# Kernel tuning notes

Hardware: AMD Instinct MI355X
Metric: run time of the kernel (lower is better)

Reference implementation:

```python
import jax, jax.numpy as jnp
import numpy as np

EPS = 1e-5
NUM_HEADS = 16
TEMP = 0.01

def _ln(x, g, b):
    m = jnp.mean(x, axis=-1, keepdims=True)
    v = jnp.var(x, axis=-1, keepdims=True)
    return (x - m) * jax.lax.rsqrt(v + EPS) * g + b

def setup_inputs() -> dict:
    key = jax.random.key(0)
    ks = jax.random.split(key, 16)
    b, l, c, ni = 4, 1024, 1024, 2
    d = c // NUM_HEADS
    s = lambda fan: 1.0 / np.sqrt(fan)
    return {
        "x_list": jax.random.normal(ks[0], (b, l, c, ni), jnp.float32),
        "w_": jax.random.normal(ks[1], (4 + ni, 1), jnp.float32),
        "qkv_w": jax.random.normal(ks[2], (3 * c, c), jnp.float32) * s(c),
        "qkv_b": jax.random.normal(ks[3], (3 * c,), jnp.float32) * 0.02,
        "proj_w": jax.random.normal(ks[4], (c, c), jnp.float32) * s(c),
        "proj_b": jax.random.normal(ks[5], (c,), jnp.float32) * 0.02,
        "nq_g": jnp.ones((d,), jnp.float32),
        "nq_b": jnp.zeros((d,), jnp.float32),
        "nk_g": jnp.ones((d,), jnp.float32),
        "nk_b": jnp.zeros((d,), jnp.float32),
        "conv_w": jax.random.normal(ks[6], (c, c), jnp.float32) * s(c),
        "conv_b": jax.random.normal(ks[7], (c,), jnp.float32) * 0.02,
        "ca1_w": jax.random.normal(ks[8], (c // 16, c), jnp.float32) * s(c),
        "ca1_b": jax.random.normal(ks[9], (c // 16,), jnp.float32) * 0.02,
        "ca2_w": jax.random.normal(ks[10], (c, c // 16), jnp.float32) * s(c // 16),
        "ca2_b": jax.random.normal(ks[11], (c,), jnp.float32) * 0.02,
        "mlp1_w": jax.random.normal(ks[12], (4 * c, c), jnp.float32) * s(c),
        "mlp1_b": jax.random.normal(ks[13], (4 * c,), jnp.float32) * 0.02,
        "mlp2_w": jax.random.normal(ks[14], (c, 4 * c), jnp.float32) * s(4 * c),
        "mlp2_b": jax.random.normal(ks[15], (c,), jnp.float32) * 0.02,
    }

def reference(x_list, w_, qkv_w, qkv_b, proj_w, proj_b, nq_g, nq_b, nk_g, nk_b,
              conv_w, conv_b, ca1_w, ca1_b, ca2_w, ca2_b, mlp1_w, mlp1_b, mlp2_w, mlp2_b):
    x = x_list[..., -1]  # [b, l, c]
    # op 0: Conv1x1Act = GELU(Linear)
    op0 = jax.nn.gelu(x @ conv_w.T + conv_b, approximate=False)
    # op 1: ChannelAttention = sigmoid(fc2(relu(fc1(x)))) * x
    op1 = jax.nn.sigmoid(jax.nn.relu(x @ ca1_w.T + ca1_b) @ ca2_w.T + ca2_b) * x
    # op 2: Identity
    op2 = x
    # op 3: MLP = fc2(GELU(fc1(x)))
    op3 = jax.nn.gelu(x @ mlp1_w.T + mlp1_b, approximate=False) @ mlp2_w.T + mlp2_b
    new = jnp.stack([op0, op1, op2, op3], axis=-1)  # [b, l, c, 4]
    xc = jnp.concatenate([x_list, new], axis=-1)    # [b, l, c, ni+4]
    w = jax.nn.softmax(w_ / TEMP, axis=0)           # [ni+4, 1]
    x = jnp.einsum('blcn,ni->blci', xc, w)[..., 0]  # [b, l, c]
    x_res = x
    # attention with per-head LayerNorm on q, k
    b_, n, c = x.shape
    d = c // NUM_HEADS
    qkv = x @ qkv_w.T + qkv_b
    q, k, v = jnp.split(qkv, 3, axis=-1)
    to_heads = lambda t: t.reshape(b_, n, NUM_HEADS, d).transpose(0, 2, 1, 3)  # [b, h, n, d]
    q, k, v = to_heads(q), to_heads(k), to_heads(v)
    q = _ln(q, nq_g, nq_b)
    k = _ln(k, nk_g, nk_b)
    score = jnp.einsum('bhnd,bhmd->bhnm', q, k) / np.sqrt(d).astype(np.float32)
    attn = jax.nn.softmax(score, axis=-1)           # [b, h, n, n]
    attn_map = attn.mean(axis=1)[:, 0, 1:]          # [b, n-1]
    out = jnp.einsum('bhnm,bhmd->bhnd', attn, v)
    out = out.transpose(0, 2, 1, 3).reshape(b_, n, c)
    out = out @ proj_w.T + proj_b + x_res
    return out, attn_map
```

## Files before the change

### kernel.cpp

```cpp
#include <hip/hip_runtime.h>
#include <hip/hip_bf16.h>

typedef __attribute__((ext_vector_type(8))) short short8;
typedef __attribute__((ext_vector_type(4))) float f32x4;

#define MROWS 4096
#define CDIM  1024
#define HEADS 16
#define DHEAD 64
#define NSEQ  1024

__device__ inline float softw(const float* __restrict__ w, int idx) {
    float m = w[0];
#pragma unroll
    for (int i = 1; i < 6; i++) m = fmaxf(m, w[i]);
    float s = 0.f, v = 0.f;
#pragma unroll
    for (int i = 0; i < 6; i++) {
        float e = __expf((w[i] - m) * 100.0f);
        s += e;
        if (i == idx) v = e;
    }
    return v / s;
}

__device__ inline float gelu_f(float x) {
    return 0.5f * x * (1.0f + erff(x * 0.70710678118654752f));
}

__global__ __launch_bounds__(256) void mix_base(
    const float* __restrict__ x_list, __hip_bfloat16* __restrict__ xb,
    float* __restrict__ am_acc)
{
    int i = blockIdx.x * 256 + threadIdx.x;
    xb[i] = __float2bfloat16(x_list[2 * (size_t)i + 1]);
    if (i < 4096) am_acc[i] = 0.f;
}

__global__ __launch_bounds__(256) void f2b(const float* __restrict__ in,
                                           __hip_bfloat16* __restrict__ out, int n)
{
    int i = blockIdx.x * 256 + threadIdx.x;
    if (i < n) out[i] = __float2bfloat16(in[i]);
}

#define BKT 32
#define LDA 40

template<int EPI, int FM, int FN>
__global__ __launch_bounds__(256) void gemm_bf16(
    const __hip_bfloat16* __restrict__ A, const __hip_bfloat16* __restrict__ W,
    const float* __restrict__ bias,
    float* __restrict__ f0, const float* __restrict__ f1,
    __hip_bfloat16* __restrict__ b0, __hip_bfloat16* __restrict__ b1,
    __hip_bfloat16* __restrict__ b2,
    const float* __restrict__ g0, const float* __restrict__ be0,
    const float* __restrict__ g1, const float* __restrict__ be1,
    const float* __restrict__ wvec, int M, int N, int K)
{
    constexpr int BMt = FM * 32;
    constexpr int BNt = FN * 32;
    constexpr int NA = BMt / 64;
    constexpr int NB = BNt / 64;
    __shared__ __hip_bfloat16 As[2][BMt * LDA];
    __shared__ __hip_bfloat16 Bs[2][BNt * LDA];
    int t = threadIdx.x;
    int n0 = blockIdx.x * BNt, m0 = blockIdx.y * BMt;
    int wave = t >> 6, lane = t & 63;
    int wr = wave >> 1, wc = wave & 1;
    int quad = lane >> 4, l16 = lane & 15;
    int r0 = t >> 2, c0 = (t & 3) * 8;

    short8 sa0[NA], sb0[NB], sa1[NA], sb1[NB];
    auto ldg = [&](int k0, short8* da, short8* db) {
#pragma unroll
        for (int i = 0; i < NA; i++)
            da[i] = *(const short8*)(A + (size_t)(m0 + r0 + 64 * i) * K + k0 + c0);
#pragma unroll
        for (int i = 0; i < NB; i++)
            db[i] = *(const short8*)(W + (size_t)(n0 + r0 + 64 * i) * K + k0 + c0);
    };
    ldg(0, sa0, sb0);
    ldg(BKT, sa1, sb1);

    f32x4 zero = {0.f, 0.f, 0.f, 0.f};
    f32x4 acc[FM][FN];
#pragma unroll
    for (int i = 0; i < FM; i++)
#pragma unroll
        for (int j = 0; j < FN; j++) acc[i][j] = zero;

    for (int k0 = 0; k0 < K; k0 += 2 * BKT) {
#pragma unroll
        for (int i = 0; i < NA; i++)
            *(short8*)&As[0][(r0 + 64 * i) * LDA + c0] = sa0[i];
#pragma unroll
        for (int i = 0; i < NB; i++)
            *(short8*)&Bs[0][(r0 + 64 * i) * LDA + c0] = sb0[i];
        __syncthreads();
        if (k0 + 2 * BKT < K) ldg(k0 + 2 * BKT, sa0, sb0);
        {
            short8 af[FM], bf[FN];
#pragma unroll
            for (int i = 0; i < FM; i++)
                af[i] = *(const short8*)&As[0][(wr * FM * 16 + i * 16 + l16) * LDA + quad * 8];
#pragma unroll
            for (int j = 0; j < FN; j++)
                bf[j] = *(const short8*)&Bs[0][(wc * FN * 16 + j * 16 + l16) * LDA + quad * 8];
#pragma unroll
            for (int i = 0; i < FM; i++)
#pragma unroll
                for (int j = 0; j < FN; j++)
                    acc[i][j] = __builtin_amdgcn_mfma_f32_16x16x32_bf16(
                        af[i], bf[j], acc[i][j], 0, 0, 0);
        }
#pragma unroll
        for (int i = 0; i < NA; i++)
            *(short8*)&As[1][(r0 + 64 * i) * LDA + c0] = sa1[i];
#pragma unroll
        for (int i = 0; i < NB; i++)
            *(short8*)&Bs[1][(r0 + 64 * i) * LDA + c0] = sb1[i];
        __syncthreads();
        if (k0 + 3 * BKT < K) ldg(k0 + 3 * BKT, sa1, sb1);
        {
            short8 af[FM], bf[FN];
#pragma unroll
            for (int i = 0; i < FM; i++)
                af[i] = *(const short8*)&As[1][(wr * FM * 16 + i * 16 + l16) * LDA + quad * 8];
#pragma unroll
            for (int j = 0; j < FN; j++)
                bf[j] = *(const short8*)&Bs[1][(wc * FN * 16 + j * 16 + l16) * LDA + quad * 8];
#pragma unroll
            for (int i = 0; i < FM; i++)
#pragma unroll
                for (int j = 0; j < FN; j++)
                    acc[i][j] = __builtin_amdgcn_mfma_f32_16x16x32_bf16(
                        af[i], bf[j], acc[i][j], 0, 0, 0);
        }
    }

    if constexpr (EPI == 1) {
        float wmx = softw(wvec, 2);
        float w0c = softw(wvec, 0);
        float w14c = softw(wvec, 1) + softw(wvec, 4);
        int colbase = n0 + wc * FN * 16;
        bool isconv = colbase < 1024;
#pragma unroll
        for (int i = 0; i < FM; i++) {
#pragma unroll
            for (int j = 0; j < FN; j++) {
                int col = colbase + j * 16 + l16;
                float bv = isconv ? bias[col] : be0[col - 1024];
#pragma unroll
                for (int r = 0; r < 4; r++) {
                    int row = m0 + wr * FM * 16 + i * 16 + quad * 4 + r;
                    float v = acc[i][j][r] + bv;
                    if (isconv) {
                        size_t idx = (size_t)row * 1024 + col;
                        float2 xl = ((const float2*)f1)[idx];
                        b0[idx] = __float2bfloat16(
                            w0c * xl.x + w14c * xl.y + wmx * gelu_f(v));
                    } else {
                        b1[(size_t)row * 4096 + (col - 1024)] =
                            __float2bfloat16(gelu_f(v));
                    }
                }
            }
        }
        return;
    }

    if constexpr (EPI == 5) {
        int colbase = n0 + wc * FN * 16;
        int portion = colbase >> 10;
        int hh = (colbase >> 6) & 15;
        float bv[FN];
#pragma unroll
        for (int j = 0; j < FN; j++) bv[j] = bias[colbase + j * 16 + l16];
        if (portion == 2) {
#pragma unroll
            for (int i = 0; i < FM; i++)
#pragma unroll
                for (int j = 0; j < FN; j++)
#pragma unroll
                    for (int r = 0; r < 4; r++) {
                        int row = m0 + wr * FM * 16 + i * 16 + quad * 4 + r;
                        int bb = row >> 10, nn = row & 1023;
                        int dd = j * 16 + l16;
                        b0[((size_t)(bb * 16 + hh) * DHEAD + dd) * NSEQ + nn] =
                            __float2bfloat16(acc[i][j][r] + bv[j]);
                    }
        } else {
            const float* g  = (portion == 0) ? g0 : g1;
            const float* be = (portion == 0) ? be0 : be1;
            __hip_bfloat16* dst = (portion == 0) ? b1 : b2;
            float gv[FN], bev[FN];
#pragma unroll
            for (int j = 0; j < FN; j++) {
                gv[j] = g[j * 16 + l16];
                bev[j] = be[j * 16 + l16];
            }
#pragma unroll
            for (int i = 0; i < FM; i++)
#pragma unroll
                for (int r = 0; r < 4; r++) {
                    float s1 = 0.f, s2 = 0.f;
#pragma unroll
                    for (int j = 0; j < FN; j++) {
                        float v = acc[i][j][r] + bv[j];
                        s1 += v; s2 += v * v;
                    }
#pragma unroll
                    for (int mk = 1; mk < 16; mk <<= 1) {
                        s1 += __shfl_xor(s1, mk, 64);
                        s2 += __shfl_xor(s2, mk, 64);
                    }
                    float mean = s1 * (1.f / 64.f);
                    float var = s2 * (1.f / 64.f) - mean * mean;
                    float rs = rsqrtf(var + 1e-5f);
                    int row = m0 + wr * FM * 16 + i * 16 + quad * 4 + r;
                    int bb = row >> 10, nn = row & 1023;
                    size_t base = ((size_t)(bb * 16 + hh) * NSEQ + nn) * DHEAD;
#pragma unroll
                    for (int j = 0; j < FN; j++)
                        dst[base + j * 16 + l16] = __float2bfloat16(
                            (acc[i][j][r] + bv[j] - mean) * rs * gv[j] + bev[j]);
                }
        }
        return;
    }

    float wmx = 0.f;
    if (EPI == 3) wmx = softw(wvec, 5);

#pragma unroll
    for (int i = 0; i < FM; i++) {
#pragma unroll
        for (int j = 0; j < FN; j++) {
            int col = n0 + wc * FN * 16 + j * 16 + l16;
            float bv = bias[col];
#pragma unroll
            for (int r = 0; r < 4; r++) {
                int row = m0 + wr * FM * 16 + i * 16 + quad * 4 + r;
                float v = acc[i][j][r] + bv;
                size_t idx = (size_t)row * N + col;
                if (EPI == 3) {
                    float tv = __bfloat162float(b0[idx]) + wmx * v;
                    b0[idx] = __float2bfloat16(tv);
                } else if (EPI == 4) {
                    f0[idx] = v + __bfloat162float(b1[idx]);
                }
            }
        }
    }
}

__global__ __launch_bounds__(256) void ca1_kernel(
    const __hip_bfloat16* __restrict__ xb, const float* __restrict__ w,
    const float* __restrict__ bias, float* __restrict__ h1)
{
    __shared__ float Xs[16 * 65];
    __shared__ float Ws[64 * 65];
    int t = threadIdx.x;
    int m0 = blockIdx.x * 16;
    int row = t >> 4, cg = t & 15;
    float acc[4] = {0.f, 0.f, 0.f, 0.f};
    for (int k0 = 0; k0 < 1024; k0 += 64) {
#pragma unroll
        for (int i = 0; i < 4; i++) {
            int e = t + i * 256; int r = e >> 6, c = e & 63;
            Xs[r * 65 + c] = __bfloat162float(xb[(size_t)(m0 + r) * 1024 + k0 + c]);
        }
#pragma unroll
        for (int i = 0; i < 16; i++) {
            int e = t + i * 256; int r = e >> 6, c = e & 63;
            Ws[r * 65 + c] = w[(size_t)r * 1024 + k0 + c];
        }
        __syncthreads();
        for (int k = 0; k < 64; k++) {
            float xv = Xs[row * 65 + k];
#pragma unroll
            for (int c = 0; c < 4; c++)
                acc[c] += xv * Ws[(cg * 4 + c) * 65 + k];
        }
        __syncthreads();
    }
#pragma unroll
    for (int c = 0; c < 4; c++)
        h1[(size_t)(m0 + row) * 64 + cg * 4 + c] =
            fmaxf(acc[c] + bias[cg * 4 + c], 0.f);
}

__global__ __launch_bounds__(256) void ca2_kernel(
    const float* __restrict__ h1, const float* __restrict__ w,
    const float* __restrict__ bias, const __hip_bfloat16* __restrict__ xb,
    __hip_bfloat16* __restrict__ xmixb, const float* __restrict__ wvec)
{
    __shared__ float Wt[256 * 65];
    __shared__ float hs[16 * 64];
    int t = threadIdx.x;
    int m0 = blockIdx.x * 16, n0 = blockIdx.y * 256;
#pragma unroll
    for (int i = 0; i < 64; i++) {
        int e = t + i * 256; int r = e >> 6, c = e & 63;
        Wt[r * 65 + c] = w[(size_t)(n0 + r) * 64 + c];
    }
#pragma unroll
    for (int i = 0; i < 4; i++) {
        int e = t + i * 256; int r = e >> 6, c = e & 63;
        hs[r * 64 + c] = h1[(size_t)(m0 + r) * 64 + c];
    }
    __syncthreads();
    int n = n0 + t;
    float bv = bias[n];
    float acc[16];
#pragma unroll
    for (int mi = 0; mi < 16; mi++) acc[mi] = bv;
    for (int k = 0; k < 64; k++) {
        float wv = Wt[t * 65 + k];
#pragma unroll
        for (int mi = 0; mi < 16; mi++) acc[mi] += hs[mi * 64 + k] * wv;
    }
    float w3 = softw(wvec, 3);
#pragma unroll
    for (int mi = 0; mi < 16; mi++) {
        size_t idx = (size_t)(m0 + mi) * 1024 + n;
        float sg = 1.f / (1.f + __expf(-acc[mi]));
        float cur = __bfloat162float(xmixb[idx]);
        xmixb[idx] = __float2bfloat16(cur + w3 * sg * __bfloat162float(xb[idx]));
    }
}

#define PSTR 72
__global__ __launch_bounds__(256) void flash_mfma(
    const __hip_bfloat16* __restrict__ qb, const __hip_bfloat16* __restrict__ kb,
    const __hip_bfloat16* __restrict__ vt, __hip_bfloat16* __restrict__ ao)
{
    __shared__ __hip_bfloat16 Plds[4][32 * PSTR];
    int bh = blockIdx.x;
    int i0 = blockIdx.y * 128;
    int b = bh >> 4, h = bh & 15;
    int t = threadIdx.x, wave = t >> 6, lane = t & 63;
    int l16 = lane & 15, quad = lane >> 4;
    const __hip_bfloat16* qbase = qb + (size_t)bh * NSEQ * DHEAD;
    const __hip_bfloat16* kbase = kb + (size_t)bh * NSEQ * DHEAD;
    const __hip_bfloat16* vbase = vt + (size_t)bh * DHEAD * NSEQ;
    __hip_bfloat16* pw = Plds[wave];
    int qrow0 = i0 + wave * 32;

    short8 aq[2][2];
#pragma unroll
    for (int ri = 0; ri < 2; ri++)
#pragma unroll
        for (int ks = 0; ks < 2; ks++)
            aq[ri][ks] = *(const short8*)(qbase +
                (size_t)(qrow0 + ri * 16 + l16) * DHEAD + ks * 32 + quad * 8);

    f32x4 zero = {0.f, 0.f, 0.f, 0.f};
    f32x4 o[2][4];
    float mrow[2][4], lrow[2][4];
#pragma unroll
    for (int ri = 0; ri < 2; ri++) {
#pragma unroll
        for (int nt = 0; nt < 4; nt++) o[ri][nt] = zero;
#pragma unroll
        for (int rr = 0; rr < 4; rr++) { mrow[ri][rr] = -1e30f; lrow[ri][rr] = 0.f; }
    }

    for (int j0 = 0; j0 < NSEQ; j0 += 64) {
        short8 bk[4][2];
#pragma unroll
        for (int jt = 0; jt < 4; jt++)
#pragma unroll
            for (int ks = 0; ks < 2; ks++)
                bk[jt][ks] = *(const short8*)(kbase +
                    (size_t)(j0 + jt * 16 + l16) * DHEAD + ks * 32 + quad * 8);
        short8 bv[4][2];
#pragma unroll
        for (int nt = 0; nt < 4; nt++)
#pragma unroll
            for (int ks = 0; ks < 2; ks++)
                bv[nt][ks] = *(const short8*)(vbase +
                    (size_t)(nt * 16 + l16) * NSEQ + j0 + ks * 32 + quad * 8);

#pragma unroll
        for (int ri = 0; ri < 2; ri++) {
            f32x4 s[4];
#pragma unroll
            for (int jt = 0; jt < 4; jt++) s[jt] = zero;
#pragma unroll
            for (int jt = 0; jt < 4; jt++)
#pragma unroll
                for (int ks = 0; ks < 2; ks++)
                    s[jt] = __builtin_amdgcn_mfma_f32_16x16x32_bf16(
                        aq[ri][ks], bk[jt][ks], s[jt], 0, 0, 0);
#pragma unroll
            for (int rr = 0; rr < 4; rr++) {
                float mx = -1e30f;
#pragma unroll
                for (int jt = 0; jt < 4; jt++) {
                    s[jt][rr] *= 0.125f;
                    mx = fmaxf(mx, s[jt][rr]);
                }
#pragma unroll
                for (int mk = 1; mk < 16; mk <<= 1) mx = fmaxf(mx, __shfl_xor(mx, mk, 64));
                float om = mrow[ri][rr];
                float nm = fmaxf(om, mx);
                float al = __expf(om - nm);
                mrow[ri][rr] = nm;
                float ss = 0.f;
#pragma unroll
                for (int jt = 0; jt < 4; jt++) {
                    float p = __expf(s[jt][rr] - nm);
                    pw[(ri * 16 + quad * 4 + rr) * PSTR + jt * 16 + l16] =
                        __float2bfloat16(p);
                    ss += p;
                }
#pragma unroll
                for (int mk = 1; mk < 16; mk <<= 1) ss += __shfl_xor(ss, mk, 64);
                lrow[ri][rr] = lrow[ri][rr] * al + ss;
#pragma unroll
                for (int nt = 0; nt < 4; nt++) o[ri][nt][rr] *= al;
            }
        }
#pragma unroll
        for (int ri = 0; ri < 2; ri++) {
            short8 ap[2];
#pragma unroll
            for (int ks = 0; ks < 2; ks++)
                ap[ks] = *(const short8*)&pw[(ri * 16 + l16) * PSTR + ks * 32 + quad * 8];
#pragma unroll
            for (int nt = 0; nt < 4; nt++)
#pragma unroll
                for (int ks = 0; ks < 2; ks++)
                    o[ri][nt] = __builtin_amdgcn_mfma_f32_16x16x32_bf16(
                        ap[ks], bv[nt][ks], o[ri][nt], 0, 0, 0);
        }
    }

#pragma unroll
    for (int ri = 0; ri < 2; ri++)
#pragma unroll
        for (int rr = 0; rr < 4; rr++) {
            float inv = 1.f / lrow[ri][rr];
            int row = qrow0 + ri * 16 + quad * 4 + rr;
#pragma unroll
            for (int nt = 0; nt < 4; nt++)
                ao[((size_t)b * NSEQ + row) * CDIM + h * 64 + nt * 16 + l16] =
                    __float2bfloat16(o[ri][nt][rr] * inv);
        }
}

__global__ __launch_bounds__(256) void attn_map_acc(
    const __hip_bfloat16* __restrict__ qf, const __hip_bfloat16* __restrict__ kf,
    float* __restrict__ am)
{
    __shared__ float q0[64];
    __shared__ float red[256];
    int bh = blockIdx.x, t = threadIdx.x;
    const __hip_bfloat16* qr = qf + (size_t)bh * NSEQ * DHEAD;
    const __hip_bfloat16* kb = kf + (size_t)bh * NSEQ * DHEAD;
    if (t < 64) q0[t] = __bfloat162float(qr[t]);
    __syncthreads();
    float s[4];
    float mx = -1e30f;
#pragma unroll
    for (int ji = 0; ji < 4; ji++) {
        int j = ji * 256 + t;
        float a = 0.f;
        for (int k = 0; k < 64; k++) a += q0[k] * __bfloat162float(kb[(size_t)j * 64 + k]);
        a *= 0.125f;
        s[ji] = a;
        mx = fmaxf(mx, a);
    }
    red[t] = mx; __syncthreads();
    for (int st = 128; st > 0; st >>= 1) {
        if (t < st) red[t] = fmaxf(red[t], red[t + st]);
        __syncthreads();
    }
    float M = red[0]; __syncthreads();
    float sum = 0.f;
#pragma unroll
    for (int ji = 0; ji < 4; ji++) { s[ji] = __expf(s[ji] - M); sum += s[ji]; }
    red[t] = sum; __syncthreads();
    for (int st = 128; st > 0; st >>= 1) {
        if (t < st) red[t] += red[t + st];
        __syncthreads();
    }
    float inv = 1.f / red[0];
    int b = bh >> 4;
#pragma unroll
    for (int ji = 0; ji < 4; ji++) {
        int j = ji * 256 + t;
        if (j > 0) atomicAdd(&am[b * 1024 + j], s[ji] * inv * (1.f / 16.f));
    }
}

__global__ __launch_bounds__(256) void attn_map_out(
    const float* __restrict__ am, float* __restrict__ out1)
{
    int i = blockIdx.x * 256 + threadIdx.x;
    if (i < 4 * 1023) {
        int b = i / 1023;
        int j = i - b * 1023 + 1;
        out1[i] = am[b * 1024 + j];
    }
}

extern "C" void kernel_launch(void* const* d_in, const int* in_sizes, int n_in,
                              void* d_out, int out_size, void* d_ws, size_t ws_size,
                              hipStream_t stream)
{
    const float* x_list = (const float*)d_in[0];
    const float* wvec   = (const float*)d_in[1];
    const float* qkv_w  = (const float*)d_in[2];
    const float* qkv_b  = (const float*)d_in[3];
    const float* proj_w = (const float*)d_in[4];
    const float* proj_b = (const float*)d_in[5];
    const float* nq_g   = (const float*)d_in[6];
    const float* nq_b   = (const float*)d_in[7];
    const float* nk_g   = (const float*)d_in[8];
    const float* nk_b   = (const float*)d_in[9];
    const float* conv_w = (const float*)d_in[10];
    const float* conv_b = (const float*)d_in[11];
    const float* ca1_w  = (const float*)d_in[12];
    const float* ca1_b  = (const float*)d_in[13];
    const float* ca2_w  = (const float*)d_in[14];
    const float* ca2_b  = (const float*)d_in[15];
    const float* mlp1_w = (const float*)d_in[16];
    const float* mlp1_b = (const float*)d_in[17];
    const float* mlp2_w = (const float*)d_in[18];
    const float* mlp2_b = (const float*)d_in[19];

    float* out0 = (float*)d_out;
    float* out1 = out0 + (size_t)4 * 1024 * 1024;

    char* ws = (char*)d_ws;
    size_t off = 0;
    auto alloc = [&](size_t bytes) -> char* {
        char* p = ws + off;
        off += (bytes + 255) & ~(size_t)255;
        return p;
    };
    __hip_bfloat16* xb     = (__hip_bfloat16*)alloc((size_t)MROWS * CDIM * 2);
    __hip_bfloat16* xmixb  = (__hip_bfloat16*)alloc((size_t)MROWS * CDIM * 2);
    float*          h1     = (float*)alloc((size_t)MROWS * 64 * 4);
    __hip_bfloat16* hb     = (__hip_bfloat16*)alloc((size_t)MROWS * 4096 * 2);
    __hip_bfloat16* qbb    = (__hip_bfloat16*)alloc((size_t)MROWS * CDIM * 2);
    __hip_bfloat16* kbb    = (__hip_bfloat16*)alloc((size_t)MROWS * CDIM * 2);
    __hip_bfloat16* vtb    = (__hip_bfloat16*)alloc((size_t)MROWS * CDIM * 2);
    __hip_bfloat16* aob    = (__hip_bfloat16*)alloc((size_t)MROWS * CDIM * 2);
    float*          amacc  = (float*)alloc(4096 * 4);
    __hip_bfloat16* wcat   = (__hip_bfloat16*)alloc((size_t)5120 * 1024 * 2);
    __hip_bfloat16* qkvwb  = (__hip_bfloat16*)alloc((size_t)3145728 * 2);
    __hip_bfloat16* projwb = (__hip_bfloat16*)alloc((size_t)1048576 * 2);
    __hip_bfloat16* mlp2wb = (__hip_bfloat16*)alloc((size_t)4194304 * 2);

    f2b<<<4096, 256, 0, stream>>>(conv_w, wcat, 1048576);
    f2b<<<16384, 256, 0, stream>>>(mlp1_w, wcat + (size_t)1048576, 4194304);
    f2b<<<12288, 256, 0, stream>>>(qkv_w, qkvwb, 3145728);
    f2b<<<4096, 256, 0, stream>>>(proj_w, projwb, 1048576);
    f2b<<<16384, 256, 0, stream>>>(mlp2_w, mlp2wb, 4194304);

    mix_base<<<16384, 256, 0, stream>>>(x_list, xb, amacc);

    gemm_bf16<1, 4, 4><<<dim3(40, 32), 256, 0, stream>>>(
        xb, wcat, conv_b, nullptr, x_list, xmixb, hb, nullptr,
        nullptr, mlp1_b, nullptr, nullptr, wvec, MROWS, 5120, 1024);

    ca1_kernel<<<256, 256, 0, stream>>>(xb, ca1_w, ca1_b, h1);
    ca2_kernel<<<dim3(256, 4), 256, 0, stream>>>(h1, ca2_w, ca2_b, xb, xmixb, wvec);

    gemm_bf16<3, 4, 4><<<dim3(8, 32), 256, 0, stream>>>(
        hb, mlp2wb, mlp2_b, nullptr, nullptr, xmixb, nullptr, nullptr,
        nullptr, nullptr, nullptr, nullptr, wvec, MROWS, 1024, 4096);

    gemm_bf16<5, 4, 4><<<dim3(24, 32), 256, 0, stream>>>(
        xmixb, qkvwb, qkv_b, nullptr, nullptr, vtb, qbb, kbb,
        nq_g, nq_b, nk_g, nk_b, wvec, MROWS, 3072, 1024);

    flash_mfma<<<dim3(64, 8), 256, 0, stream>>>(qbb, kbb, vtb, aob);

    attn_map_acc<<<64, 256, 0, stream>>>(qbb, kbb, amacc);
    attn_map_out<<<16, 256, 0, stream>>>(amacc, out1);

    gemm_bf16<4, 4, 4><<<dim3(8, 32), 256, 0, stream>>>(
        aob, projwb, proj_b, out0, nullptr, nullptr, xmixb, nullptr,
        nullptr, nullptr, nullptr, nullptr, wvec, MROWS, 1024, 1024);
}
```

Measured before the change: 548.4 us.

## Fuse weight/input conversion kernels, fuse channel-attention stages, widen first GEMM tile

Merges the five weight fp32-to-bf16 conversions and the input extraction into a single vectorized prep kernel, cutting launch count and using float4 loads. Fuses the two channel-attention kernels into one so the hidden activations stay in shared memory instead of making a global round trip. Changes the first GEMM tile from 4x4 to 4x8 fragments, halving its grid. The fused CA kernel has only 256 blocks, each looping over all output columns serially, which may reduce parallelism compared with the previous 1024-block second stage.

New measurement: 703.5 us. 1.28x slower.

```diff
diff --git a/kernel.cpp b/kernel.cpp
--- a/kernel.cpp
+++ b/kernel.cpp
@@ -28,20 +28,46 @@
     return 0.5f * x * (1.0f + erff(x * 0.70710678118654752f));
 }
 
-__global__ __launch_bounds__(256) void mix_base(
-    const float* __restrict__ x_list, __hip_bfloat16* __restrict__ xb,
-    float* __restrict__ am_acc)
+#define S0 1048576ULL
+#define S1 (S0 + 4194304ULL)
+#define S2 (S1 + 3145728ULL)
+#define S3 (S2 + 1048576ULL)
+#define S4 (S3 + 4194304ULL)
+#define S5 (S4 + 4194304ULL)
+
+__global__ __launch_bounds__(256) void prep_all(
+    const float* __restrict__ conv_w, const float* __restrict__ mlp1_w,
+    const float* __restrict__ qkv_w, const float* __restrict__ proj_w,
+    const float* __restrict__ mlp2_w, const float* __restrict__ x_list,
+    __hip_bfloat16* __restrict__ wcat, __hip_bfloat16* __restrict__ qkvwb,
+    __hip_bfloat16* __restrict__ projwb, __hip_bfloat16* __restrict__ mlp2wb,
+    __hip_bfloat16* __restrict__ xb, float* __restrict__ amacc)
 {
-    int i = blockIdx.x * 256 + threadIdx.x;
-    xb[i] = __float2bfloat16(x_list[2 * (size_t)i + 1]);
-    if (i < 4096) am_acc[i] = 0.f;
-}
-
-__global__ __launch_bounds__(256) void f2b(const float* __restrict__ in,
-                                           __hip_bfloat16* __restrict__ out, int n)
-{
-    int i = blockIdx.x * 256 + threadIdx.x;
-    if (i < n) out[i] = __float2bfloat16(in[i]);
+    size_t gid = (size_t)blockIdx.x * 256 + threadIdx.x;
+    if (gid < 4096) amacc[gid] = 0.f;
+    size_t i = gid * 4;
+    if (i >= S5) return;
+    float4 v;
+    __hip_bfloat16* d;
+    if (i < S4) {
+        const float* src;
+        if (i < S0)      { src = conv_w + i;        d = wcat + i; }
+        else if (i < S1) { src = mlp1_w + (i - S0); d = wcat + i; }
+        else if (i < S2) { src = qkv_w + (i - S1);  d = qkvwb + (i - S1); }
+        else if (i < S3) { src = proj_w + (i - S2); d = projwb + (i - S2); }
+        else             { src = mlp2_w + (i - S3); d = mlp2wb + (i - S3); }
+        v = *(const float4*)src;
+    } else {
+        size_t j = i - S4;
+        const float4* xp = (const float4*)(x_list + 2 * j);
+        float4 a = xp[0], b = xp[1];
+        v.x = a.y; v.y = a.w; v.z = b.y; v.w = b.w;
+        d = xb + j;
+    }
+    d[0] = __float2bfloat16(v.x);
+    d[1] = __float2bfloat16(v.y);
+    d[2] = __float2bfloat16(v.z);
+    d[3] = __float2bfloat16(v.w);
 }
 
 #define BKT 32
@@ -255,16 +281,21 @@
     }
 }
 
-__global__ __launch_bounds__(256) void ca1_kernel(
-    const __hip_bfloat16* __restrict__ xb, const float* __restrict__ w,
-    const float* __restrict__ bias, float* __restrict__ h1)
+__global__ __launch_bounds__(256) void ca_fused(
+    const __hip_bfloat16* __restrict__ xb, const float* __restrict__ w1,
+    const float* __restrict__ b1, const float* __restrict__ w2,
+    const float* __restrict__ b2, __hip_bfloat16* __restrict__ xmixb,
+    const float* __restrict__ wvec)
 {
-    __shared__ float Xs[16 * 65];
-    __shared__ float Ws[64 * 65];
+    __shared__ float S[16640 + 16 * 64];
+    float* Xs = S;
+    float* Ws = S + 1040;
+    float* hs = S + 16640;
+    float* Wt = S;
     int t = threadIdx.x;
     int m0 = blockIdx.x * 16;
     int row = t >> 4, cg = t & 15;
-    float acc[4] = {0.f, 0.f, 0.f, 0.f};
+    float acc1[4] = {0.f, 0.f, 0.f, 0.f};
     for (int k0 = 0; k0 < 1024; k0 += 64) {
 #pragma unroll
         for (int i = 0; i < 4; i++) {
@@ -274,60 +305,47 @@
 #pragma unroll
         for (int i = 0; i < 16; i++) {
             int e = t + i * 256; int r = e >> 6, c = e & 63;
-            Ws[r * 65 + c] = w[(size_t)r * 1024 + k0 + c];
+            Ws[r * 65 + c] = w1[(size_t)r * 1024 + k0 + c];
         }
         __syncthreads();
         for (int k = 0; k < 64; k++) {
             float xv = Xs[row * 65 + k];
 #pragma unroll
             for (int c = 0; c < 4; c++)
-                acc[c] += xv * Ws[(cg * 4 + c) * 65 + k];
+                acc1[c] += xv * Ws[(cg * 4 + c) * 65 + k];
         }
         __syncthreads();
     }
 #pragma unroll
     for (int c = 0; c < 4; c++)
-        h1[(size_t)(m0 + row) * 64 + cg * 4 + c] =
-            fmaxf(acc[c] + bias[cg * 4 + c], 0.f);
-}
-
-__global__ __launch_bounds__(256) void ca2_kernel(
-    const float* __restrict__ h1, const float* __restrict__ w,
-    const float* __restrict__ bias, const __hip_bfloat16* __restrict__ xb,
-    __hip_bfloat16* __restrict__ xmixb, const float* __restrict__ wvec)
-{
-    __shared__ float Wt[256 * 65];
-    __shared__ float hs[16 * 64];
-    int t = threadIdx.x;
-    int m0 = blockIdx.x * 16, n0 = blockIdx.y * 256;
-#pragma unroll
-    for (int i = 0; i < 64; i++) {
-        int e = t + i * 256; int r = e >> 6, c = e & 63;
-        Wt[r * 65 + c] = w[(size_t)(n0 + r) * 64 + c];
-    }
-#pragma unroll
-    for (int i = 0; i < 4; i++) {
-        int e = t + i * 256; int r = e >> 6, c = e & 63;
-        hs[r * 64 + c] = h1[(size_t)(m0 + r) * 64 + c];
-    }
-    __syncthreads();
-    int n = n0 + t;
-    float bv = bias[n];
-    float acc[16];
-#pragma unroll
-    for (int mi = 0; mi < 16; mi++) acc[mi] = bv;
-    for (int k = 0; k < 64; k++) {
-        float wv = Wt[t * 65 + k];
-#pragma unroll
-        for (int mi = 0; mi < 16; mi++) acc[mi] += hs[mi * 64 + k] * wv;
-    }
+        hs[row * 64 + cg * 4 + c] = fmaxf(acc1[c] + b1[cg * 4 + c], 0.f);
+
     float w3 = softw(wvec, 3);
-#pragma unroll
-    for (int mi = 0; mi < 16; mi++) {
-        size_t idx = (size_t)(m0 + mi) * 1024 + n;
-        float sg = 1.f / (1.f + __expf(-acc[mi]));
-        float cur = __bfloat162float(xmixb[idx]);
-        xmixb[idx] = __float2bfloat16(cur + w3 * sg * __bfloat162float(xb[idx]));
+    for (int n0 = 0; n0 < 1024; n0 += 256) {
+        __syncthreads();
+#pragma unroll
+        for (int i = 0; i < 64; i++) {
+            int e = t + i * 256; int r = e >> 6, c = e & 63;
+            Wt[r * 65 + c] = w2[(size_t)(n0 + r) * 64 + c];
+        }
+        __syncthreads();
+        int n = n0 + t;
+        float bv = b2[n];
+        float acc[16];
+#pragma unroll
+        for (int mi = 0; mi < 16; mi++) acc[mi] = bv;
+        for (int k = 0; k < 64; k++) {
+            float wv = Wt[t * 65 + k];
+#pragma unroll
+            for (int mi = 0; mi < 16; mi++) acc[mi] += hs[mi * 64 + k] * wv;
+        }
+#pragma unroll
+        for (int mi = 0; mi < 16; mi++) {
+            size_t idx = (size_t)(m0 + mi) * 1024 + n;
+            float sg = 1.f / (1.f + __expf(-acc[mi]));
+            float cur = __bfloat162float(xmixb[idx]);
+            xmixb[idx] = __float2bfloat16(cur + w3 * sg * __bfloat162float(xb[idx]));
+        }
     }
 }
 
@@ -544,7 +562,6 @@
     };
     __hip_bfloat16* xb     = (__hip_bfloat16*)alloc((size_t)MROWS * CDIM * 2);
     __hip_bfloat16* xmixb  = (__hip_bfloat16*)alloc((size_t)MROWS * CDIM * 2);
-    float*          h1     = (float*)alloc((size_t)MROWS * 64 * 4);
     __hip_bfloat16* hb     = (__hip_bfloat16*)alloc((size_t)MROWS * 4096 * 2);
     __hip_bfloat16* qbb    = (__hip_bfloat16*)alloc((size_t)MROWS * CDIM * 2);
     __hip_bfloat16* kbb    = (__hip_bfloat16*)alloc((size_t)MROWS * CDIM * 2);
@@ -556,20 +573,15 @@
     __hip_bfloat16* projwb = (__hip_bfloat16*)alloc((size_t)1048576 * 2);
     __hip_bfloat16* mlp2wb = (__hip_bfloat16*)alloc((size_t)4194304 * 2);
 
-    f2b<<<4096, 256, 0, stream>>>(conv_w, wcat, 1048576);
-    f2b<<<16384, 256, 0, stream>>>(mlp1_w, wcat + (size_t)1048576, 4194304);
-    f2b<<<12288, 256, 0, stream>>>(qkv_w, qkvwb, 3145728);
-    f2b<<<4096, 256, 0, stream>>>(proj_w, projwb, 1048576);
-    f2b<<<16384, 256, 0, stream>>>(mlp2_w, mlp2wb, 4194304);
-
-    mix_base<<<16384, 256, 0, stream>>>(x_list, xb, amacc);
-
-    gemm_bf16<1, 4, 4><<<dim3(40, 32), 256, 0, stream>>>(
+    prep_all<<<17408, 256, 0, stream>>>(
+        conv_w, mlp1_w, qkv_w, proj_w, mlp2_w, x_list,
+        wcat, qkvwb, projwb, mlp2wb, xb, amacc);
+
+    gemm_bf16<1, 4, 8><<<dim3(20, 32), 256, 0, stream>>>(
         xb, wcat, conv_b, nullptr, x_list, xmixb, hb, nullptr,
         nullptr, mlp1_b, nullptr, nullptr, wvec, MROWS, 5120, 1024);
 
-    ca1_kernel<<<256, 256, 0, stream>>>(xb, ca1_w, ca1_b, h1);
-    ca2_kernel<<<dim3(256, 4), 256, 0, stream>>>(h1, ca2_w, ca2_b, xb, xmixb, wvec);
+    ca_fused<<<256, 256, 0, stream>>>(xb, ca1_w, ca1_b, ca2_w, ca2_b, xmixb, wvec);
 
     gemm_bf16<3, 4, 4><<<dim3(8, 32), 256, 0, stream>>>(
         hb, mlp2wb, mlp2_b, nullptr, nullptr, xmixb, nullptr, nullptr,
```
